# Kernel optimization log

Measured on AMD Instinct MI355X. Metric: run time of the kernel, lower is better.

The kernel has to match this reference:

```python
import jax, jax.numpy as jnp
import numpy as np
import math

B, T, C, H = 4, 2048, 1024, 16
EPS = 1e-10

def setup_inputs() -> dict:
    key = jax.random.key(0)
    ks = jax.random.split(key, 9)
    s = 0.02
    return {
        "x": jax.random.normal(ks[0], (B, T, C), jnp.float32),
        "w_attn": jax.random.normal(ks[1], (3 * C, C), jnp.float32) * s,
        "b_attn": jax.random.normal(ks[2], (3 * C,), jnp.float32) * s,
        "w_proj": jax.random.normal(ks[3], (C, C), jnp.float32) * s,
        "b_proj": jax.random.normal(ks[4], (C,), jnp.float32) * s,
        "w_fc": jax.random.normal(ks[5], (4 * C, C), jnp.float32) * s,
        "b_fc": jax.random.normal(ks[6], (4 * C,), jnp.float32) * s,
        "w_mlp_proj": jax.random.normal(ks[7], (C, 4 * C), jnp.float32) * s,
        "b_mlp_proj": jax.random.normal(ks[8], (C,), jnp.float32) * s,
    }

def layernorm(x):
    # custom LayerNormalization: no gamma/beta, eps=1e-10, biased variance
    mean = jnp.mean(x, axis=-1, keepdims=True)
    xmu = x - mean
    var = jnp.mean(xmu * xmu, axis=-1, keepdims=True)
    return xmu / jnp.sqrt(var + EPS)

def new_gelu(x):
    # 0.5*x*(1+tanh(sqrt(2/pi)*(x+0.044715*x^3)))
    c = math.sqrt(2.0 / math.pi)
    return 0.5 * x * (1.0 + jnp.tanh(c * (x + 0.044715 * x * x * x)))

def attention(x, w_attn, b_attn, w_proj, b_proj):
    b, t, cdim = x.shape
    d = cdim // H
    ca = x @ w_attn.T + b_attn                      # [B,T,3C]
    q, k, v = jnp.split(ca, 3, axis=2)
    q = q.reshape(b, t, H, d)
    k = k.reshape(b, t, H, d)
    v = v.reshape(b, t, H, d)
    att = jnp.einsum('bthd,bshd->bhts', q, k) * (1.0 / math.sqrt(d))
    mask = jnp.tril(jnp.ones((t, t), dtype=bool))
    att = jnp.where(mask, att, -jnp.inf)
    att = jax.nn.softmax(att, axis=-1)
    y = jnp.einsum('bhts,bshd->bthd', att, v).reshape(b, t, cdim)
    return y @ w_proj.T + b_proj

def reference(x, w_attn, b_attn, w_proj, b_proj, w_fc, b_fc, w_mlp_proj, b_mlp_proj):
    x = x + attention(layernorm(x), w_attn, b_attn, w_proj, b_proj)
    h = new_gelu(layernorm(x) @ w_fc.T + b_fc)
    x = x + (h @ w_mlp_proj.T + b_mlp_proj)
    return x
```

## Files before the change

### kernel.cpp

```cpp
#include <hip/hip_runtime.h>
#include <math.h>

constexpr int Bb = 4;
constexpr int Tt = 2048;
constexpr int Cc = 1024;
constexpr int Hh = 16;
constexpr int Dh = 64;
constexpr int Mm = Bb * Tt;

typedef __attribute__((ext_vector_type(8))) short s16x8;
typedef __attribute__((ext_vector_type(4))) short s16x4;
typedef __attribute__((ext_vector_type(4))) float f32x4;

__device__ __forceinline__ unsigned short f2bf(float x) {
    unsigned u = __float_as_uint(x);
    u += 0x7FFFu + ((u >> 16) & 1u);
    return (unsigned short)(u >> 16);
}
__device__ __forceinline__ float bf2f(unsigned short h) {
    return __uint_as_float((unsigned)h << 16);
}

__device__ __forceinline__ void gld16(const void* g, void* l) {
    __builtin_amdgcn_global_load_lds(
        (const __attribute__((address_space(1))) void*)g,
        (__attribute__((address_space(3))) void*)l, 16, 0, 0);
}


__global__ __launch_bounds__(256) void ln_conv_kernel(const float* __restrict__ in,
                                                      char* __restrict__ out) {
    const int row = blockIdx.x;
    const float4 v = reinterpret_cast<const float4*>(in + (size_t)row * Cc)[threadIdx.x];
    float s = v.x + v.y + v.z + v.w;
    float q = v.x * v.x + v.y * v.y + v.z * v.z + v.w * v.w;
#pragma unroll
    for (int off = 32; off > 0; off >>= 1) {
        s += __shfl_xor(s, off);
        q += __shfl_xor(q, off);
    }
    __shared__ float red[2][4];
    const int wid = threadIdx.x >> 6;
    if ((threadIdx.x & 63) == 0) { red[0][wid] = s; red[1][wid] = q; }
    __syncthreads();
    s = red[0][0] + red[0][1] + red[0][2] + red[0][3];
    q = red[1][0] + red[1][1] + red[1][2] + red[1][3];
    const float mean = s * (1.0f / Cc);
    const float var = q * (1.0f / Cc) - mean * mean;
    const float rstd = rsqrtf(var + 1e-10f);
    float o[4] = {(v.x - mean) * rstd, (v.y - mean) * rstd,
                  (v.z - mean) * rstd, (v.w - mean) * rstd};
    s16x4 hv, lv;
#pragma unroll
    for (int j = 0; j < 4; ++j) {
        unsigned short h = f2bf(o[j]);
        hv[j] = (short)h;
        lv[j] = (short)f2bf(o[j] - bf2f(h));
    }
    const int c0 = threadIdx.x * 4;
    char* p = out + (size_t)row * 4096 + ((c0 >> 5) * 8 + ((c0 >> 3) & 3)) * 16 + (c0 & 7) * 2;
    *reinterpret_cast<s16x4*>(p) = hv;
    *reinterpret_cast<s16x4*>(p + 64) = lv;
}

__global__ __launch_bounds__(256) void wconv_kernel(const float* __restrict__ W,
                                                    char* __restrict__ out,
                                                    int noct, int oshift, int ldk) {
    const int idx = blockIdx.x * 256 + threadIdx.x;
    if (idx >= noct) return;
    const int r = idx >> oshift;
    const int oct = idx & ((1 << oshift) - 1);
    const float* p = W + (size_t)r * ldk + oct * 8;
    float4 a = *reinterpret_cast<const float4*>(p);
    float4 b = *reinterpret_cast<const float4*>(p + 4);
    float xs[8] = {a.x, a.y, a.z, a.w, b.x, b.y, b.z, b.w};
    s16x8 hv, lv;
#pragma unroll
    for (int j = 0; j < 8; ++j) {
        unsigned short h = f2bf(xs[j]);
        hv[j] = (short)h;
        lv[j] = (short)f2bf(xs[j] - bf2f(h));
    }
    const int Kg = 1 << (oshift - 2);
    char* o = out + (((size_t)r * Kg + (oct >> 2)) * 8 + (oct & 3)) * 16;
    *reinterpret_cast<s16x8*>(o) = hv;
    *reinterpret_cast<s16x8*>(o + 64) = lv;
}

__device__ __forceinline__ float gelu_f(float v) {
    const float z = 1.5957691216057308f * (v + 0.044715f * v * v * v);
    return v / (1.0f + __expf(-z));
}

template <bool GELU, bool RESID, bool CONVOUT, bool ADDBIAS>
__global__ __launch_bounds__(512, 2) void gemm_mfma8(
    const char* __restrict__ Ac, const char* __restrict__ Bc,
    const float* __restrict__ bias, const float* __restrict__ resid,
    float* __restrict__ Cout, char* __restrict__ Cconv,
    int M, int N, int K) {
    const int tid = threadIdx.x;
    const int lane = tid & 63;
    const int wid = tid >> 6;
    const int gx = gridDim.x;
    const int nwg = gx * gridDim.y;
    int flat = blockIdx.y * gx + blockIdx.x;
    flat = (flat & 7) * (nwg >> 3) + (flat >> 3);
    const int bn = (flat % gx) * 256;
    const int bm = (flat / gx) * 256;
    const int wm = (wid >> 2) * 128;
    const int wn = (wid & 3) * 64;
    const int Kg = K >> 5;

    __shared__ char lds[131072];

    f32x4 acc[8][4];
#pragma unroll
    for (int i = 0; i < 8; ++i)
#pragma unroll
        for (int j = 0; j < 4; ++j) acc[i][j] = (f32x4)0.0f;

    unsigned int aoff[4], boff[4], ldso[4];
#pragma unroll
    for (int i = 0; i < 4; ++i) {
        const int u = tid + i * 512;
        const int r = u >> 3;
        const int s = (u & 7) ^ (r & 7);
        aoff[i] = (unsigned int)((bm + r) * Kg * 128 + s * 16);
        boff[i] = (unsigned int)((bn + r) * Kg * 128 + s * 16);
        ldso[i] = (unsigned int)(u * 16);
    }

    const int g = lane >> 4, fr = lane & 15;
    unsigned int afo[8], bfo[4];
#pragma unroll
    for (int i = 0; i < 8; ++i) {
        const int ra = wm + i * 16 + fr;
        afo[i] = (unsigned int)(ra * 128 + ((g ^ (ra & 7)) << 4));
    }
#pragma unroll
    for (int j = 0; j < 4; ++j) {
        const int rb = wn + j * 16 + fr;
        bfo[j] = (unsigned int)(rb * 128 + ((g ^ (rb & 7)) << 4));
    }

    auto stage = [&](int tt, int buf) {
        char* Ad = lds + buf * 65536;
        char* Bd = Ad + 32768;
        const unsigned int tb = (unsigned int)tt * 128;
#pragma unroll
        for (int i = 0; i < 4; ++i) gld16(Ac + aoff[i] + tb, Ad + ldso[i]);
#pragma unroll
        for (int i = 0; i < 4; ++i) gld16(Bc + boff[i] + tb, Bd + ldso[i]);
    };

    stage(0, 0);
    asm volatile("s_waitcnt vmcnt(0)" ::: "memory");
    __builtin_amdgcn_s_barrier();

    s16x8 Bh[4], Bl[4];
    for (int t = 0; t < Kg; ++t) {
        const int c = t & 1;
        const char* Ab = lds + c * 65536;
        const char* Bb = Ab + 32768;
#pragma unroll
        for (int q = 0; q < 4; ++q) {
            if (q == 0) {
#pragma unroll
                for (int j = 0; j < 4; ++j) {
                    Bh[j] = *reinterpret_cast<const s16x8*>(Bb + bfo[j]);
                    Bl[j] = *reinterpret_cast<const s16x8*>(Bb + (bfo[j] ^ 64u));
                }
            }
            const s16x8 Ah0 = *reinterpret_cast<const s16x8*>(Ab + afo[2 * q]);
            const s16x8 Al0 = *reinterpret_cast<const s16x8*>(Ab + (afo[2 * q] ^ 64u));
            const s16x8 Ah1 = *reinterpret_cast<const s16x8*>(Ab + afo[2 * q + 1]);
            const s16x8 Al1 = *reinterpret_cast<const s16x8*>(Ab + (afo[2 * q + 1] ^ 64u));
            if (q == 0 && t + 1 < Kg) stage(t + 1, c ^ 1);
            __builtin_amdgcn_s_barrier();
            asm volatile("s_waitcnt lgkmcnt(0)" ::: "memory");
            __builtin_amdgcn_sched_barrier(0);
            __builtin_amdgcn_s_setprio(1);
#pragma unroll
            for (int j = 0; j < 4; ++j) {
                acc[2 * q][j] = __builtin_amdgcn_mfma_f32_16x16x32_bf16(Ah0, Bh[j], acc[2 * q][j], 0, 0, 0);
                acc[2 * q][j] = __builtin_amdgcn_mfma_f32_16x16x32_bf16(Al0, Bh[j], acc[2 * q][j], 0, 0, 0);
                acc[2 * q][j] = __builtin_amdgcn_mfma_f32_16x16x32_bf16(Ah0, Bl[j], acc[2 * q][j], 0, 0, 0);
                acc[2 * q + 1][j] = __builtin_amdgcn_mfma_f32_16x16x32_bf16(Ah1, Bh[j], acc[2 * q + 1][j], 0, 0, 0);
                acc[2 * q + 1][j] = __builtin_amdgcn_mfma_f32_16x16x32_bf16(Al1, Bh[j], acc[2 * q + 1][j], 0, 0, 0);
                acc[2 * q + 1][j] = __builtin_amdgcn_mfma_f32_16x16x32_bf16(Ah1, Bl[j], acc[2 * q + 1][j], 0, 0, 0);
            }
            __builtin_amdgcn_s_setprio(0);
            __builtin_amdgcn_sched_barrier(0);
            if (q == 3) asm volatile("s_waitcnt vmcnt(0)" ::: "memory");
            __builtin_amdgcn_s_barrier();
        }
    }

    float bcol[4];
#pragma unroll
    for (int j = 0; j < 4; ++j)
        bcol[j] = ADDBIAS ? bias[bn + wn + j * 16 + fr] : 0.0f;

#pragma unroll
    for (int i = 0; i < 8; ++i) {
#pragma unroll
        for (int rr = 0; rr < 4; ++rr) {
            const int row = bm + wm + i * 16 + g * 4 + rr;
#pragma unroll
            for (int j = 0; j < 4; ++j) {
                const int col = bn + wn + j * 16 + fr;
                float v = acc[i][j][rr] + bcol[j];
                if (RESID) v += resid[(size_t)row * N + col];
                if (GELU) v = gelu_f(v);
                if (!CONVOUT) {
                    Cout[(size_t)row * N + col] = v;
                } else {
                    const unsigned short h = f2bf(v);
                    const unsigned short l = f2bf(v - bf2f(h));
                    char* p = Cconv +
                              (((size_t)row * (N >> 5) + (col >> 5)) * 8 + ((col >> 3) & 3)) * 16 +
                              (col & 7) * 2;
                    *reinterpret_cast<unsigned short*>(p) = h;
                    *reinterpret_cast<unsigned short*>(p + 64) = l;
                }
            }
        }
    }
}

__global__ __launch_bounds__(256) void qkv_repack_kernel(
    const float* __restrict__ qkv, unsigned short* __restrict__ qb,
    unsigned short* __restrict__ kb, unsigned short* __restrict__ vtb) {
    const int bh = blockIdx.y;
    const int b = bh >> 4, h = bh & 15;
    const int t0 = blockIdx.x * 64;
    const int tid = threadIdx.x;
    __shared__ unsigned short vtile[64][66];
#pragma unroll
    for (int r = 0; r < 16; ++r) {
        const int idx = tid + r * 256;
        const int t = idx >> 6, d = idx & 63;
        const size_t src = (size_t)(b * Tt + t0 + t) * 3072 + h * 64 + d;
        const size_t dst = ((size_t)bh * Tt + t0 + t) * 64 + d;
        qb[dst] = f2bf(qkv[src] * 0.125f);
        kb[dst] = f2bf(qkv[src + 1024]);
        vtile[t][d] = f2bf(qkv[src + 2048]);
    }
    __syncthreads();
#pragma unroll
    for (int r = 0; r < 16; ++r) {
        const int idx = tid + r * 256;
        const int d = idx >> 6, t = idx & 63;
        vtb[((size_t)bh * 64 + d) * Tt + t0 + t] = vtile[t][d];
    }
}

__global__ __launch_bounds__(256) void attn_mfma_kernel(
    const unsigned short* __restrict__ qbuf, const unsigned short* __restrict__ kbuf,
    const unsigned short* __restrict__ vtbuf, char* __restrict__ yconv) {
    const int qt = blockIdx.x;
    const int bh = blockIdx.y;
    const int tid = threadIdx.x;
    const int w = tid >> 6, lane = tid & 63;
    const int g = lane >> 4, fr = lane & 15;
    const int qbase = qt * 64;

    const unsigned short* Q  = qbuf  + (size_t)bh * Tt * 64;
    const unsigned short* K  = kbuf  + (size_t)bh * Tt * 64;
    const unsigned short* Vt = vtbuf + (size_t)bh * 64 * Tt;

    __shared__ unsigned short Kl[64][72];
    __shared__ unsigned short Vl[64][72];
    __shared__ unsigned short Pl[4][16][72];

    s16x8 qf[2];
#pragma unroll
    for (int s = 0; s < 2; ++s)
        qf[s] = *reinterpret_cast<const s16x8*>(
            &Q[(size_t)(qbase + 16 * w + fr) * 64 + s * 32 + 8 * g]);

    f32x4 acc_o[4];
#pragma unroll
    for (int jd = 0; jd < 4; ++jd) acc_o[jd] = (f32x4)0.0f;
    float lpart[4] = {0.f, 0.f, 0.f, 0.f};

    for (int t0 = 0; t0 <= qt; ++t0) {
        __syncthreads();
#pragma unroll
        for (int r2 = 0; r2 < 2; ++r2) {
            const int idx = tid + r2 * 256;
            const int row = idx >> 3, c = idx & 7;
            *reinterpret_cast<s16x8*>(&Kl[row][c * 8]) =
                *reinterpret_cast<const s16x8*>(&K[(size_t)(t0 * 64 + row) * 64 + c * 8]);
            *reinterpret_cast<s16x8*>(&Vl[row][c * 8]) =
                *reinterpret_cast<const s16x8*>(&Vt[(size_t)row * Tt + t0 * 64 + c * 8]);
        }
        __syncthreads();

        f32x4 acc_s[4];
#pragma unroll
        for (int jk = 0; jk < 4; ++jk) acc_s[jk] = (f32x4)0.0f;
#pragma unroll
        for (int s = 0; s < 2; ++s)
#pragma unroll
            for (int jk = 0; jk < 4; ++jk) {
                const s16x8 kf = *reinterpret_cast<const s16x8*>(
                    &Kl[16 * jk + fr][s * 32 + 8 * g]);
                acc_s[jk] = __builtin_amdgcn_mfma_f32_16x16x32_bf16(qf[s], kf, acc_s[jk], 0, 0, 0);
            }

        const bool diag = (t0 == qt);
#pragma unroll
        for (int jk = 0; jk < 4; ++jk)
#pragma unroll
            for (int rr = 0; rr < 4; ++rr) {
                const int key = 16 * jk + fr;
                const int qrow = 16 * w + 4 * g + rr;
                float p = __expf(acc_s[jk][rr]);
                if (diag && key > qrow) p = 0.0f;
                lpart[rr] += p;
                Pl[w][4 * g + rr][key] = f2bf(p);
            }

#pragma unroll
        for (int s = 0; s < 2; ++s) {
            const s16x8 pf = *reinterpret_cast<const s16x8*>(&Pl[w][fr][s * 32 + 8 * g]);
#pragma unroll
            for (int jd = 0; jd < 4; ++jd) {
                const s16x8 vf = *reinterpret_cast<const s16x8*>(
                    &Vl[16 * jd + fr][s * 32 + 8 * g]);
                acc_o[jd] = __builtin_amdgcn_mfma_f32_16x16x32_bf16(pf, vf, acc_o[jd], 0, 0, 0);
            }
        }
    }

#pragma unroll
    for (int rr = 0; rr < 4; ++rr) {
#pragma unroll
        for (int off = 1; off < 16; off <<= 1)
            lpart[rr] += __shfl_xor(lpart[rr], off);
    }
    float inv[4];
#pragma unroll
    for (int rr = 0; rr < 4; ++rr) inv[rr] = 1.0f / lpart[rr];

    const int bq = bh >> 4;
#pragma unroll
    for (int rr = 0; rr < 4; ++rr) {
        const int row = bq * Tt + qbase + 16 * w + 4 * g + rr;
#pragma unroll
        for (int jd = 0; jd < 4; ++jd) {
            const int col = (bh & 15) * Dh + 16 * jd + fr;
            const float v = acc_o[jd][rr] * inv[rr];
            const unsigned short h = f2bf(v);
            const unsigned short l = f2bf(v - bf2f(h));
            char* p = yconv + (((size_t)row * (Cc >> 5) + (col >> 5)) * 8 + ((col >> 3) & 3)) * 16 +
                      (col & 7) * 2;
            *reinterpret_cast<unsigned short*>(p) = h;
            *reinterpret_cast<unsigned short*>(p + 64) = l;
        }
    }
}

extern "C" void kernel_launch(void* const* d_in, const int* in_sizes, int n_in,
                              void* d_out, int out_size, void* d_ws,
                              size_t ws_size, hipStream_t stream) {
    const float* x      = (const float*)d_in[0];
    const float* w_attn = (const float*)d_in[1];
    const float* b_attn = (const float*)d_in[2];
    const float* w_proj = (const float*)d_in[3];
    const float* b_proj = (const float*)d_in[4];
    const float* w_fc   = (const float*)d_in[5];
    const float* b_fc   = (const float*)d_in[6];
    const float* w_mlp  = (const float*)d_in[7];
    const float* b_mlp  = (const float*)d_in[8];
    float* out = (float*)d_out;

    if (ws_size < (176ull << 20)) return;

    char* ws = (char*)d_ws;
    char*  slotbuf = ws;
    float* qkv     = (float*)(ws + (32ull << 20));
    char*  hconv   = ws + (32ull << 20);
    unsigned short* qb = (unsigned short*)(ws + (128ull << 20));
    unsigned short* kb = (unsigned short*)(ws + (144ull << 20));
    unsigned short* vt = (unsigned short*)(ws + (160ull << 20));
    char*  wscr    = ws + (160ull << 20);
    float* x1      = out;

    ln_conv_kernel<<<Mm, 256, 0, stream>>>(x, slotbuf);
    wconv_kernel<<<1536, 256, 0, stream>>>(w_attn, wscr, 3072 * 128, 7, 1024);
    gemm_mfma8<false, false, false, true><<<dim3(12, 32), 512, 0, stream>>>(
        slotbuf, wscr, b_attn, nullptr, qkv, nullptr, Mm, 3 * Cc, Cc);
    qkv_repack_kernel<<<dim3(Tt / 64, Bb * Hh), 256, 0, stream>>>(qkv, qb, kb, vt);
    attn_mfma_kernel<<<dim3(Tt / 64, Bb * Hh), 256, 0, stream>>>(qb, kb, vt, slotbuf);
    wconv_kernel<<<512, 256, 0, stream>>>(w_proj, wscr, 1024 * 128, 7, 1024);
    gemm_mfma8<false, true, false, true><<<dim3(4, 32), 512, 0, stream>>>(
        slotbuf, wscr, b_proj, x, x1, nullptr, Mm, Cc, Cc);
    ln_conv_kernel<<<Mm, 256, 0, stream>>>(x1, slotbuf);
    wconv_kernel<<<2048, 256, 0, stream>>>(w_fc, wscr, 4096 * 128, 7, 1024);
    gemm_mfma8<true, false, true, true><<<dim3(16, 32), 512, 0, stream>>>(
        slotbuf, wscr, b_fc, nullptr, nullptr, hconv, Mm, 4 * Cc, Cc);
    wconv_kernel<<<2048, 256, 0, stream>>>(w_mlp, wscr, 1024 * 512, 9, 4096);
    gemm_mfma8<false, true, false, true><<<dim3(4, 32), 512, 0, stream>>>(
        hconv, wscr, b_mlp, x1, out, nullptr, Mm, Cc, 4 * Cc);
}
```

Baseline: 996.9 us.

## Shrink GEMM tile to 256x128 and use triple-buffered LDS prefetch

The GEMM tile shrinks from 256x256 to 256x128, which doubles the grid size for every GEMM launch and halves the accumulators per wave. The LDS pipeline goes from double to triple buffering: stages are issued two K-steps ahead, and the global loads are spread across the q sub-iterations. The wait now uses a partial vmcnt instead of a full drain each step. The aim is more workgroups to fill the CUs and better hiding of load latency. In exchange, each tile reuses data less, and the 144KB of LDS likely limits occupancy to one block per CU despite launch_bounds(512,2).

```diff
diff --git a/kernel.cpp b/kernel.cpp
--- a/kernel.cpp
+++ b/kernel.cpp
@@ -105,95 +105,123 @@
     const int nwg = gx * gridDim.y;
     int flat = blockIdx.y * gx + blockIdx.x;
     flat = (flat & 7) * (nwg >> 3) + (flat >> 3);
-    const int bn = (flat % gx) * 256;
+    const int bn = (flat % gx) * 128;
     const int bm = (flat / gx) * 256;
-    const int wm = (wid >> 2) * 128;
-    const int wn = (wid & 3) * 64;
+    const int wm = (wid >> 1) * 64;
+    const int wn = (wid & 1) * 64;
     const int Kg = K >> 5;
 
-    __shared__ char lds[131072];
-
-    f32x4 acc[8][4];
-#pragma unroll
-    for (int i = 0; i < 8; ++i)
+    __shared__ char lds[147456];
+
+    f32x4 acc[4][4];
+#pragma unroll
+    for (int i = 0; i < 4; ++i)
 #pragma unroll
         for (int j = 0; j < 4; ++j) acc[i][j] = (f32x4)0.0f;
 
-    unsigned int aoff[4], boff[4], ldso[4];
+    unsigned int aoff[4], boff[2], ldsoA[4], ldsoB[2];
 #pragma unroll
     for (int i = 0; i < 4; ++i) {
         const int u = tid + i * 512;
         const int r = u >> 3;
         const int s = (u & 7) ^ (r & 7);
         aoff[i] = (unsigned int)((bm + r) * Kg * 128 + s * 16);
+        ldsoA[i] = (unsigned int)(u * 16);
+    }
+#pragma unroll
+    for (int i = 0; i < 2; ++i) {
+        const int u = tid + i * 512;
+        const int r = u >> 3;
+        const int s = (u & 7) ^ (r & 7);
         boff[i] = (unsigned int)((bn + r) * Kg * 128 + s * 16);
-        ldso[i] = (unsigned int)(u * 16);
+        ldsoB[i] = (unsigned int)(32768 + u * 16);
     }
 
     const int g = lane >> 4, fr = lane & 15;
-    unsigned int afo[8], bfo[4];
-#pragma unroll
-    for (int i = 0; i < 8; ++i) {
+    unsigned int afo[4], bfo[4];
+#pragma unroll
+    for (int i = 0; i < 4; ++i) {
         const int ra = wm + i * 16 + fr;
         afo[i] = (unsigned int)(ra * 128 + ((g ^ (ra & 7)) << 4));
     }
 #pragma unroll
     for (int j = 0; j < 4; ++j) {
         const int rb = wn + j * 16 + fr;
-        bfo[j] = (unsigned int)(rb * 128 + ((g ^ (rb & 7)) << 4));
-    }
-
-    auto stage = [&](int tt, int buf) {
-        char* Ad = lds + buf * 65536;
-        char* Bd = Ad + 32768;
-        const unsigned int tb = (unsigned int)tt * 128;
-#pragma unroll
-        for (int i = 0; i < 4; ++i) gld16(Ac + aoff[i] + tb, Ad + ldso[i]);
-#pragma unroll
-        for (int i = 0; i < 4; ++i) gld16(Bc + boff[i] + tb, Bd + ldso[i]);
-    };
-
-    stage(0, 0);
-    asm volatile("s_waitcnt vmcnt(0)" ::: "memory");
-    __builtin_amdgcn_s_barrier();
-
-    s16x8 Bh[4], Bl[4];
+        bfo[j] = (unsigned int)(32768 + rb * 128 + ((g ^ (rb & 7)) << 4));
+    }
+
+    {
+        char* d0 = lds;
+        char* d1 = lds + 49152;
+#pragma unroll
+        for (int i = 0; i < 4; ++i) gld16(Ac + aoff[i], d0 + ldsoA[i]);
+#pragma unroll
+        for (int i = 0; i < 2; ++i) gld16(Bc + boff[i], d0 + ldsoB[i]);
+        if (Kg > 1) {
+#pragma unroll
+            for (int i = 0; i < 4; ++i) gld16(Ac + aoff[i] + 128, d1 + ldsoA[i]);
+#pragma unroll
+            for (int i = 0; i < 2; ++i) gld16(Bc + boff[i] + 128, d1 + ldsoB[i]);
+            asm volatile("s_waitcnt vmcnt(6)" ::: "memory");
+        } else {
+            asm volatile("s_waitcnt vmcnt(0)" ::: "memory");
+        }
+        __builtin_amdgcn_s_barrier();
+    }
+
+    int cbuf = 0;
+    int sbuf = 2;
     for (int t = 0; t < Kg; ++t) {
-        const int c = t & 1;
-        const char* Ab = lds + c * 65536;
-        const char* Bb = Ab + 32768;
+        const char* Ab = lds + cbuf * 49152;
+        const bool pf = (t + 2 < Kg);
+        char* Sd = lds + sbuf * 49152;
+        const unsigned int tb2 = (unsigned int)(t + 2) * 128;
+
+        s16x8 Bh[4], Bl[4];
 #pragma unroll
         for (int q = 0; q < 4; ++q) {
             if (q == 0) {
 #pragma unroll
                 for (int j = 0; j < 4; ++j) {
-                    Bh[j] = *reinterpret_cast<const s16x8*>(Bb + bfo[j]);
-                    Bl[j] = *reinterpret_cast<const s16x8*>(Bb + (bfo[j] ^ 64u));
+                    Bh[j] = *reinterpret_cast<const s16x8*>(Ab + bfo[j]);
+                    Bl[j] = *reinterpret_cast<const s16x8*>(Ab + (bfo[j] ^ 64u));
                 }
             }
-            const s16x8 Ah0 = *reinterpret_cast<const s16x8*>(Ab + afo[2 * q]);
-            const s16x8 Al0 = *reinterpret_cast<const s16x8*>(Ab + (afo[2 * q] ^ 64u));
-            const s16x8 Ah1 = *reinterpret_cast<const s16x8*>(Ab + afo[2 * q + 1]);
-            const s16x8 Al1 = *reinterpret_cast<const s16x8*>(Ab + (afo[2 * q + 1] ^ 64u));
-            if (q == 0 && t + 1 < Kg) stage(t + 1, c ^ 1);
+            const s16x8 Ah = *reinterpret_cast<const s16x8*>(Ab + afo[q]);
+            const s16x8 Al = *reinterpret_cast<const s16x8*>(Ab + (afo[q] ^ 64u));
+            if (pf) {
+                if (q == 0) {
+                    gld16(Ac + aoff[0] + tb2, Sd + ldsoA[0]);
+                    gld16(Ac + aoff[1] + tb2, Sd + ldsoA[1]);
+                } else if (q == 1) {
+                    gld16(Ac + aoff[2] + tb2, Sd + ldsoA[2]);
+                    gld16(Ac + aoff[3] + tb2, Sd + ldsoA[3]);
+                } else if (q == 2) {
+                    gld16(Bc + boff[0] + tb2, Sd + ldsoB[0]);
+                    gld16(Bc + boff[1] + tb2, Sd + ldsoB[1]);
+                }
+            }
             __builtin_amdgcn_s_barrier();
             asm volatile("s_waitcnt lgkmcnt(0)" ::: "memory");
             __builtin_amdgcn_sched_barrier(0);
             __builtin_amdgcn_s_setprio(1);
 #pragma unroll
             for (int j = 0; j < 4; ++j) {
-                acc[2 * q][j] = __builtin_amdgcn_mfma_f32_16x16x32_bf16(Ah0, Bh[j], acc[2 * q][j], 0, 0, 0);
-                acc[2 * q][j] = __builtin_amdgcn_mfma_f32_16x16x32_bf16(Al0, Bh[j], acc[2 * q][j], 0, 0, 0);
-                acc[2 * q][j] = __builtin_amdgcn_mfma_f32_16x16x32_bf16(Ah0, Bl[j], acc[2 * q][j], 0, 0, 0);
-                acc[2 * q + 1][j] = __builtin_amdgcn_mfma_f32_16x16x32_bf16(Ah1, Bh[j], acc[2 * q + 1][j], 0, 0, 0);
-                acc[2 * q + 1][j] = __builtin_amdgcn_mfma_f32_16x16x32_bf16(Al1, Bh[j], acc[2 * q + 1][j], 0, 0, 0);
-                acc[2 * q + 1][j] = __builtin_amdgcn_mfma_f32_16x16x32_bf16(Ah1, Bl[j], acc[2 * q + 1][j], 0, 0, 0);
+                acc[q][j] = __builtin_amdgcn_mfma_f32_16x16x32_bf16(Ah, Bh[j], acc[q][j], 0, 0, 0);
+                acc[q][j] = __builtin_amdgcn_mfma_f32_16x16x32_bf16(Al, Bh[j], acc[q][j], 0, 0, 0);
+                acc[q][j] = __builtin_amdgcn_mfma_f32_16x16x32_bf16(Ah, Bl[j], acc[q][j], 0, 0, 0);
             }
             __builtin_amdgcn_s_setprio(0);
-            __builtin_amdgcn_sched_barrier(0);
-            if (q == 3) asm volatile("s_waitcnt vmcnt(0)" ::: "memory");
+            if (q == 3 && t + 1 < Kg) {
+                if (pf)
+                    asm volatile("s_waitcnt vmcnt(6)" ::: "memory");
+                else
+                    asm volatile("s_waitcnt vmcnt(0)" ::: "memory");
+            }
             __builtin_amdgcn_s_barrier();
         }
+        cbuf = (cbuf == 2) ? 0 : cbuf + 1;
+        sbuf = (sbuf == 2) ? 0 : sbuf + 1;
     }
 
     float bcol[4];
@@ -202,7 +230,7 @@
         bcol[j] = ADDBIAS ? bias[bn + wn + j * 16 + fr] : 0.0f;
 
 #pragma unroll
-    for (int i = 0; i < 8; ++i) {
+    for (int i = 0; i < 4; ++i) {
 #pragma unroll
         for (int rr = 0; rr < 4; ++rr) {
             const int row = bm + wm + i * 16 + g * 4 + rr;
@@ -390,18 +418,18 @@
 
     ln_conv_kernel<<<Mm, 256, 0, stream>>>(x, slotbuf);
     wconv_kernel<<<1536, 256, 0, stream>>>(w_attn, wscr, 3072 * 128, 7, 1024);
-    gemm_mfma8<false, false, false, true><<<dim3(12, 32), 512, 0, stream>>>(
+    gemm_mfma8<false, false, false, true><<<dim3(24, 32), 512, 0, stream>>>(
         slotbuf, wscr, b_attn, nullptr, qkv, nullptr, Mm, 3 * Cc, Cc);
     qkv_repack_kernel<<<dim3(Tt / 64, Bb * Hh), 256, 0, stream>>>(qkv, qb, kb, vt);
     attn_mfma_kernel<<<dim3(Tt / 64, Bb * Hh), 256, 0, stream>>>(qb, kb, vt, slotbuf);
     wconv_kernel<<<512, 256, 0, stream>>>(w_proj, wscr, 1024 * 128, 7, 1024);
-    gemm_mfma8<false, true, false, true><<<dim3(4, 32), 512, 0, stream>>>(
+    gemm_mfma8<false, true, false, true><<<dim3(8, 32), 512, 0, stream>>>(
         slotbuf, wscr, b_proj, x, x1, nullptr, Mm, Cc, Cc);
     ln_conv_kernel<<<Mm, 256, 0, stream>>>(x1, slotbuf);
     wconv_kernel<<<2048, 256, 0, stream>>>(w_fc, wscr, 4096 * 128, 7, 1024);
-    gemm_mfma8<true, false, true, true><<<dim3(16, 32), 512, 0, stream>>>(
+    gemm_mfma8<true, false, true, true><<<dim3(32, 32), 512, 0, stream>>>(
         slotbuf, wscr, b_fc, nullptr, nullptr, hconv, Mm, 4 * Cc, Cc);
     wconv_kernel<<<2048, 256, 0, stream>>>(w_mlp, wscr, 1024 * 512, 9, 4096);
-    gemm_mfma8<false, true, false, true><<<dim3(4, 32), 512, 0, stream>>>(
+    gemm_mfma8<false, true, false, true><<<dim3(8, 32), 512, 0, stream>>>(
         hconv, wscr, b_mlp, x1, out, nullptr, Mm, Cc, 4 * Cc);
 }
```

Result: faster. 922.5 us (-7.5%).
